# Kernel optimization log

Hardware: AMD Instinct MI355X
Metric: run time of the kernel (lower is better)

The kernel has to match this reference:

```python
import jax, jax.numpy as jnp
import numpy as np

EPS = 1e-6


def setup_inputs() -> dict:
    key = jax.random.key(0)
    k1, _ = jax.random.split(key)
    L, D = 128, 262144
    slots = jax.random.normal(k1, (L, D), dtype=jnp.float32)
    temperature = jnp.ones((), dtype=jnp.float32)  # temperature = 1.0
    return {"slots": slots, "temperature": temperature, "length": L}


def reference(slots, temperature, length):
    # slots: [L, D]; pairwise cosine similarity (torch: x.y / max(|x||y|, eps))
    L = length
    norms = jnp.sqrt(jnp.sum(slots * slots, axis=1))                # [L]
    gram = jnp.einsum('id,jd->ij', slots, slots)                    # [L, L]
    sim = gram / jnp.maximum(norms[:, None] * norms[None, :], EPS)  # [L, L]
    logits = sim / temperature
    E = jnp.exp(logits)                                             # [L, L]
    # denominator for pair (i, j): sum_{k != j} exp(sim(i,k)/T)  (k=i included)
    denom = jnp.sum(E, axis=1, keepdims=True) - E                   # [L, L]
    log_ratio = logits - jnp.log(denom)                             # log(num/den)
    idx = jnp.arange(L)
    penalty = jnp.abs(idx[:, None] - idx[None, :]).astype(slots.dtype)  # |i-j|
    upper = (idx[:, None] < idx[None, :]).astype(slots.dtype)           # i < j
    total = jnp.sum(-log_ratio * penalty * upper)
    # original divides by i*j/2 with final loop values i=j=length-1
    total = total / ((L - 1) * (L - 1) / 2.0)
    return total
```

## Files before the change

kernel.cpp:

```cpp
#include <hip/hip_runtime.h>
#include <hip/hip_bf16.h>

typedef __attribute__((ext_vector_type(8))) short bf16x8;
typedef __attribute__((ext_vector_type(4))) float f32x4;

constexpr int L  = 128;
constexpr int BK = 64;
constexpr int GRID = 512;

__device__ inline float blo(unsigned w) { unsigned v = w << 16;          return __builtin_bit_cast(float, v); }
__device__ inline float bhi(unsigned w) { unsigned v = w & 0xffff0000u;  return __builtin_bit_cast(float, v); }

__global__ __launch_bounds__(256, 2)
void gram_kernel(const float* __restrict__ slots, unsigned* __restrict__ p16,
                 unsigned* __restrict__ counter, int D, int nChunks, int G) {
    __shared__ __align__(16) float lbuf[2][L * BK];
    const int t    = threadIdx.x;
    const int wave = t >> 6;
    const int lane = t & 63;

    if (blockIdx.x == 0 && t == 0) *counter = 0;

    f32x4 acc[2][8];
#pragma unroll
    for (int r = 0; r < 2; ++r)
#pragma unroll
        for (int c = 0; c < 8; ++c) acc[r][c] = (f32x4)0.f;

    auto stage = [&](int buf, int chunk) {
        const size_t cbyte = (size_t)chunk * (BK * 4);
#pragma unroll
        for (int q = 0; q < 8; ++q) {
            const int rowidx = (wave * 8 + q) * 4 + (lane >> 4);
            const int gu     = (lane & 15) ^ (rowidx & 15);
            const char* src  = (const char*)slots +
                               (size_t)rowidx * D * 4 + cbyte + (size_t)gu * 16;
            __builtin_amdgcn_global_load_lds(
                (const __attribute__((address_space(1))) unsigned*)src,
                (__attribute__((address_space(3))) unsigned*)&lbuf[buf][(wave * 8 + q) * 256],
                16, 0, 0);
        }
    };

    auto ldfrag = [&](const float* base, int row, int kk) -> bf16x8 {
        const int u0 = (kk >> 2) + ((lane >> 4) << 1);
        const int p0 = u0 ^ (row & 15);
        const int p1 = (u0 + 1) ^ (row & 15);
        const f32x4 f0 = *reinterpret_cast<const f32x4*>(base + row * BK + p0 * 4);
        const f32x4 f1 = *reinterpret_cast<const f32x4*>(base + row * BK + p1 * 4);
        const unsigned* a = reinterpret_cast<const unsigned*>(&f0);
        const unsigned* b = reinterpret_cast<const unsigned*>(&f1);
        union { bf16x8 v; unsigned w[4]; } r;
        r.w[0] = __builtin_amdgcn_perm(a[1], a[0], 0x07060302u);
        r.w[1] = __builtin_amdgcn_perm(a[3], a[2], 0x07060302u);
        r.w[2] = __builtin_amdgcn_perm(b[1], b[0], 0x07060302u);
        r.w[3] = __builtin_amdgcn_perm(b[3], b[2], 0x07060302u);
        return r.v;
    };

    stage(0, blockIdx.x);
    __syncthreads();

    int k = 0;
    for (int c = blockIdx.x; c < nChunks; c += G, ++k) {
        const int cur = k & 1;
        if (c + G < nChunks) stage(cur ^ 1, c + G);

#pragma unroll
        for (int kk = 0; kk < BK; kk += 32) {
            bf16x8 a0 = ldfrag(&lbuf[cur][0], wave * 32 +      (lane & 15), kk);
            bf16x8 a1 = ldfrag(&lbuf[cur][0], wave * 32 + 16 + (lane & 15), kk);
#pragma unroll
            for (int cc = 0; cc < 8; ++cc) {
                bf16x8 b = ldfrag(&lbuf[cur][0], cc * 16 + (lane & 15), kk);
                acc[0][cc] = __builtin_amdgcn_mfma_f32_16x16x32_bf16(a0, b, acc[0][cc], 0, 0, 0);
                acc[1][cc] = __builtin_amdgcn_mfma_f32_16x16x32_bf16(a1, b, acc[1][cc], 0, 0, 0);
            }
        }
        __syncthreads();
    }

    unsigned* pb = p16 + (size_t)blockIdx.x * 8192;
#pragma unroll
    for (int r = 0; r < 2; ++r)
#pragma unroll
        for (int c = 0; c < 8; ++c) {
            const unsigned* a = reinterpret_cast<const unsigned*>(&acc[r][c]);
            uint2 w;
            w.x = __builtin_amdgcn_perm(a[1], a[0], 0x07060302u);
            w.y = __builtin_amdgcn_perm(a[3], a[2], 0x07060302u);
            *reinterpret_cast<uint2*>(pb + (((r * 8 + c) * 256 + t) << 1)) = w;
        }
}

__global__ __launch_bounds__(256)
void reduce_finalize(const unsigned* __restrict__ p16, float* __restrict__ gram,
                     unsigned* __restrict__ counter,
                     const float* __restrict__ temperature, float* __restrict__ out,
                     int G) {
    __shared__ f32x4 red[8][32];
    __shared__ float norms[L];
    __shared__ float wred[4];
    __shared__ unsigned ticket_s;
    const int t   = threadIdx.x;
    const int sub = t >> 5;
    const int sl  = t & 31;
    const int j   = blockIdx.x * 32 + sl;

    const uint2* pt2 = reinterpret_cast<const uint2*>(p16);
    f32x4 s = (f32x4)0.f;
#pragma unroll 8
    for (int b = sub; b < G; b += 8) {
        const uint2 u = pt2[(size_t)b * 4096 + j];
        s[0] += blo(u.x); s[1] += bhi(u.x);
        s[2] += blo(u.y); s[3] += bhi(u.y);
    }
    red[sub][sl] = s;
    __syncthreads();
    if (t < 32) {
        f32x4 s4 = red[0][t];
#pragma unroll
        for (int w = 1; w < 8; ++w) s4 += red[w][t];
        const int myj  = blockIdx.x * 32 + t;
        const int slot = myj >> 8, tenc = myj & 255;
        const int wv = tenc >> 6, ln = tenc & 63;
        const int r = slot >> 3, c = slot & 7;
        const int growb = wv * 32 + r * 16 + ((ln >> 4) << 2);
        const int gcol  = c * 16 + (ln & 15);
#pragma unroll
        for (int q = 0; q < 4; ++q) gram[(growb + q) * L + gcol] = s4[q];
    }

    __syncthreads();
    if (t == 0) {
        __threadfence();
        ticket_s = atomicAdd(counter, 1u);
    }
    __syncthreads();
    if (ticket_s != (unsigned)(gridDim.x - 1)) return;
    __threadfence();

    if (t < L) norms[t] = sqrtf(gram[t * L + t]);
    __syncthreads();

    const float invT = 1.0f / temperature[0];
    const int r = t >> 1;
    const int q = t & 1;
    const float ni = norms[r];

    float ps = 0.f;
    for (int jj = q; jj < L; jj += 2) {
        float sim = gram[r * L + jj] / fmaxf(ni * norms[jj], 1e-6f);
        ps += __expf(sim * invT);
    }
    ps += __shfl_xor(ps, 1);
    const float rowsum = ps;

    float tot = 0.f;
    for (int jj = q; jj < L; jj += 2) {
        if (jj > r) {
            float logit = (gram[r * L + jj] / fmaxf(ni * norms[jj], 1e-6f)) * invT;
            tot += -(logit - __logf(rowsum - __expf(logit))) * (float)(jj - r);
        }
    }
#pragma unroll
    for (int m = 1; m < 64; m <<= 1) tot += __shfl_xor(tot, m);
    if ((t & 63) == 0) wred[t >> 6] = tot;
    __syncthreads();
    if (t == 0)
        out[0] = (wred[0] + wred[1] + wred[2] + wred[3]) /
                 ((float)(L - 1) * (float)(L - 1) * 0.5f);
}

extern "C" void kernel_launch(void* const* d_in, const int* in_sizes, int n_in,
                              void* d_out, int out_size, void* d_ws, size_t ws_size,
                              hipStream_t stream) {
    const float* slots       = (const float*)d_in[0];
    const float* temperature = (const float*)d_in[1];
    float* out  = (float*)d_out;

    const int D = in_sizes[0] / L;
    const int nChunks = D / BK;
    int G = GRID;
    if (G > nChunks) G = nChunks;

    unsigned* p16     = (unsigned*)d_ws;
    float*    gram    = (float*)((char*)d_ws + (size_t)G * 32768);
    unsigned* counter = (unsigned*)((char*)gram + (size_t)L * L * 4);

    gram_kernel<<<G, 256, 0, stream>>>(slots, p16, counter, D, nChunks, G);
    reduce_finalize<<<128, 256, 0, stream>>>(p16, gram, counter, temperature, out, G);
}
```

Before: 59.60 us.

## Stage slots via registers as bf16 into swizzled LDS with 512-thread blocks

New measurement: 58.87 us. Within noise of the previous version (-1.2%).

```diff
diff --git a/kernel.cpp b/kernel.cpp
--- a/kernel.cpp
+++ b/kernel.cpp
@@ -4,97 +4,96 @@
 typedef __attribute__((ext_vector_type(8))) short bf16x8;
 typedef __attribute__((ext_vector_type(4))) float f32x4;
 
-constexpr int L  = 128;
-constexpr int BK = 64;
-constexpr int GRID = 512;
+constexpr int L     = 128;
+constexpr int BK    = 64;
+constexpr int GRID  = 512;
+constexpr int PITCH = BK * 2;
 
 __device__ inline float blo(unsigned w) { unsigned v = w << 16;          return __builtin_bit_cast(float, v); }
 __device__ inline float bhi(unsigned w) { unsigned v = w & 0xffff0000u;  return __builtin_bit_cast(float, v); }
 
-__global__ __launch_bounds__(256, 2)
-void gram_kernel(const float* __restrict__ slots, unsigned* __restrict__ p16,
+__global__ __launch_bounds__(512, 4)
+void gram_kernel(const float* __restrict__ slots, uint2* __restrict__ p16,
                  unsigned* __restrict__ counter, int D, int nChunks, int G) {
-    __shared__ __align__(16) float lbuf[2][L * BK];
+    __shared__ __align__(16) char lds[2][L * PITCH];
     const int t    = threadIdx.x;
     const int wave = t >> 6;
     const int lane = t & 63;
 
     if (blockIdx.x == 0 && t == 0) *counter = 0;
 
-    f32x4 acc[2][8];
+    f32x4 acc[8];
 #pragma unroll
-    for (int r = 0; r < 2; ++r)
+    for (int c = 0; c < 8; ++c) acc[c] = (f32x4)0.f;
+
+    float4 ld[4];
+
+    auto issue = [&](int chunk) {
 #pragma unroll
-        for (int c = 0; c < 8; ++c) acc[r][c] = (f32x4)0.f;
-
-    auto stage = [&](int buf, int chunk) {
-        const size_t cbyte = (size_t)chunk * (BK * 4);
-#pragma unroll
-        for (int q = 0; q < 8; ++q) {
-            const int rowidx = (wave * 8 + q) * 4 + (lane >> 4);
-            const int gu     = (lane & 15) ^ (rowidx & 15);
-            const char* src  = (const char*)slots +
-                               (size_t)rowidx * D * 4 + cbyte + (size_t)gu * 16;
-            __builtin_amdgcn_global_load_lds(
-                (const __attribute__((address_space(1))) unsigned*)src,
-                (__attribute__((address_space(3))) unsigned*)&lbuf[buf][(wave * 8 + q) * 256],
-                16, 0, 0);
+        for (int q = 0; q < 4; ++q) {
+            int idx  = t + 512 * q;
+            int row  = idx >> 4;
+            int col4 = idx & 15;
+            ld[q] = *reinterpret_cast<const float4*>(
+                slots + (size_t)row * D + (size_t)chunk * BK + col4 * 4);
         }
     };
-
-    auto ldfrag = [&](const float* base, int row, int kk) -> bf16x8 {
-        const int u0 = (kk >> 2) + ((lane >> 4) << 1);
-        const int p0 = u0 ^ (row & 15);
-        const int p1 = (u0 + 1) ^ (row & 15);
-        const f32x4 f0 = *reinterpret_cast<const f32x4*>(base + row * BK + p0 * 4);
-        const f32x4 f1 = *reinterpret_cast<const f32x4*>(base + row * BK + p1 * 4);
-        const unsigned* a = reinterpret_cast<const unsigned*>(&f0);
-        const unsigned* b = reinterpret_cast<const unsigned*>(&f1);
-        union { bf16x8 v; unsigned w[4]; } r;
-        r.w[0] = __builtin_amdgcn_perm(a[1], a[0], 0x07060302u);
-        r.w[1] = __builtin_amdgcn_perm(a[3], a[2], 0x07060302u);
-        r.w[2] = __builtin_amdgcn_perm(b[1], b[0], 0x07060302u);
-        r.w[3] = __builtin_amdgcn_perm(b[3], b[2], 0x07060302u);
-        return r.v;
+    auto commit = [&](int buf) {
+#pragma unroll
+        for (int q = 0; q < 4; ++q) {
+            int idx  = t + 512 * q;
+            int row  = idx >> 4;
+            int col4 = idx & 15;
+            const unsigned* f = reinterpret_cast<const unsigned*>(&ld[q]);
+            uint2 w;
+            w.x = __builtin_amdgcn_perm(f[1], f[0], 0x07060302u);
+            w.y = __builtin_amdgcn_perm(f[3], f[2], 0x07060302u);
+            int byte = (col4 * 8) ^ ((row & 7) << 4);
+            *reinterpret_cast<uint2*>(&lds[buf][row * PITCH + byte]) = w;
+        }
+    };
+    auto ldfrag = [&](int buf, int row, int kk) -> bf16x8 {
+        int byte = row * PITCH + ((kk * 2 + ((lane >> 4) << 4)) ^ ((row & 7) << 4));
+        return *reinterpret_cast<const bf16x8*>(&lds[buf][byte]);
     };
 
-    stage(0, blockIdx.x);
+    issue(blockIdx.x);
+    commit(0);
     __syncthreads();
 
     int k = 0;
     for (int c = blockIdx.x; c < nChunks; c += G, ++k) {
         const int cur = k & 1;
-        if (c + G < nChunks) stage(cur ^ 1, c + G);
+        const bool more = (c + G < nChunks);
+        if (more) issue(c + G);
 
 #pragma unroll
         for (int kk = 0; kk < BK; kk += 32) {
-            bf16x8 a0 = ldfrag(&lbuf[cur][0], wave * 32 +      (lane & 15), kk);
-            bf16x8 a1 = ldfrag(&lbuf[cur][0], wave * 32 + 16 + (lane & 15), kk);
+            bf16x8 a = ldfrag(cur, wave * 16 + (lane & 15), kk);
 #pragma unroll
             for (int cc = 0; cc < 8; ++cc) {
-                bf16x8 b = ldfrag(&lbuf[cur][0], cc * 16 + (lane & 15), kk);
-                acc[0][cc] = __builtin_amdgcn_mfma_f32_16x16x32_bf16(a0, b, acc[0][cc], 0, 0, 0);
-                acc[1][cc] = __builtin_amdgcn_mfma_f32_16x16x32_bf16(a1, b, acc[1][cc], 0, 0, 0);
+                bf16x8 b = ldfrag(cur, cc * 16 + (lane & 15), kk);
+                acc[cc] = __builtin_amdgcn_mfma_f32_16x16x32_bf16(a, b, acc[cc], 0, 0, 0);
             }
         }
+
+        if (more) commit(cur ^ 1);
         __syncthreads();
     }
 
-    unsigned* pb = p16 + (size_t)blockIdx.x * 8192;
+    uint2* pb = p16 + (size_t)blockIdx.x * 4096;
 #pragma unroll
-    for (int r = 0; r < 2; ++r)
-#pragma unroll
-        for (int c = 0; c < 8; ++c) {
-            const unsigned* a = reinterpret_cast<const unsigned*>(&acc[r][c]);
-            uint2 w;
-            w.x = __builtin_amdgcn_perm(a[1], a[0], 0x07060302u);
-            w.y = __builtin_amdgcn_perm(a[3], a[2], 0x07060302u);
-            *reinterpret_cast<uint2*>(pb + (((r * 8 + c) * 256 + t) << 1)) = w;
-        }
+    for (int cc = 0; cc < 8; ++cc) {
+        const unsigned* a = reinterpret_cast<const unsigned*>(&acc[cc]);
+        uint2 w;
+        w.x = __builtin_amdgcn_perm(a[1], a[0], 0x07060302u);
+        w.y = __builtin_amdgcn_perm(a[3], a[2], 0x07060302u);
+        pb[cc * 512 + t] = w;
+    }
 }
 
 __global__ __launch_bounds__(256)
-void reduce_finalize(const unsigned* __restrict__ p16, float* __restrict__ gram,
+void reduce_finalize(const uint2* __restrict__ p16, float* __restrict__ gram,
                      unsigned* __restrict__ counter,
                      const float* __restrict__ temperature, float* __restrict__ out,
                      int G) {
@@ -107,11 +106,10 @@
     const int sl  = t & 31;
     const int j   = blockIdx.x * 32 + sl;
 
-    const uint2* pt2 = reinterpret_cast<const uint2*>(p16);
     f32x4 s = (f32x4)0.f;
 #pragma unroll 8
     for (int b = sub; b < G; b += 8) {
-        const uint2 u = pt2[(size_t)b * 4096 + j];
+        const uint2 u = p16[(size_t)b * 4096 + j];
         s[0] += blo(u.x); s[1] += bhi(u.x);
         s[2] += blo(u.y); s[3] += bhi(u.y);
     }
@@ -122,11 +120,11 @@
 #pragma unroll
         for (int w = 1; w < 8; ++w) s4 += red[w][t];
         const int myj  = blockIdx.x * 32 + t;
-        const int slot = myj >> 8, tenc = myj & 255;
+        const int cc   = myj >> 9;
+        const int tenc = myj & 511;
         const int wv = tenc >> 6, ln = tenc & 63;
-        const int r = slot >> 3, c = slot & 7;
-        const int growb = wv * 32 + r * 16 + ((ln >> 4) << 2);
-        const int gcol  = c * 16 + (ln & 15);
+        const int growb = wv * 16 + ((ln >> 4) << 2);
+        const int gcol  = cc * 16 + (ln & 15);
 #pragma unroll
         for (int q = 0; q < 4; ++q) gram[(growb + q) * L + gcol] = s4[q];
     }
@@ -184,10 +182,10 @@
     int G = GRID;
     if (G > nChunks) G = nChunks;
 
-    unsigned* p16     = (unsigned*)d_ws;
+    uint2*    p16     = (uint2*)d_ws;
     float*    gram    = (float*)((char*)d_ws + (size_t)G * 32768);
     unsigned* counter = (unsigned*)((char*)gram + (size_t)L * L * 4);
 
-    gram_kernel<<<G, 256, 0, stream>>>(slots, p16, counter, D, nChunks, G);
+    gram_kernel<<<G, 512, 0, stream>>>(slots, p16, counter, D, nChunks, G);
     reduce_finalize<<<128, 256, 0, stream>>>(p16, gram, counter, temperature, out, G);
 }
```
